# Performance work log

Hardware: AMD Instinct MI355X
Metric: run time of the kernel (lower is better)

Reference implementation:

```python
import jax, jax.numpy as jnp
import numpy as np

GAMMA = 267.52  # gyromagnetic ratio constant used as default in forward


def make_laplacian_kernel(vox=(1.0, 1.0, 1.0)):
    vx, vy, vz = vox
    mx, my, mz = 1.0 / vx ** 2, 1.0 / vy ** 2, 1.0 / vz ** 2
    mv = -2.0 * (mx + my + mz)
    k = np.zeros((3, 3, 3), dtype=np.float32)
    # layout matches the torch conv_op nested list: k[d, h, w]
    k[0, 1, 1] = mz
    k[2, 1, 1] = mz
    k[1, 0, 1] = mx
    k[1, 2, 1] = mx
    k[1, 1, 0] = my
    k[1, 1, 2] = my
    k[1, 1, 1] = mv
    return jnp.asarray(k)[None, None]  # [O=1, I=1, 3, 3, 3]


def lg(x, kernel):
    # conv3d, stride 1, padding 1 (SAME for 3^3 kernel), NCDHW
    out = jax.lax.conv_general_dilated(
        x, kernel, window_strides=(1, 1, 1), padding=[(1, 1)] * 3,
        dimension_numbers=('NCDHW', 'OIDHW', 'NCDHW'))
    # zero the boundary slices along each spatial dim (matches LG)
    out = out.at[:, :, 0, :, :].set(0.0).at[:, :, -1, :, :].set(0.0)
    out = out.at[:, :, :, 0, :].set(0.0).at[:, :, :, -1, :].set(0.0)
    out = out.at[:, :, :, :, 0].set(0.0).at[:, :, :, :, -1].set(0.0)
    return out


def setup_inputs() -> dict:
    key = jax.random.key(0)
    k1, k2 = jax.random.split(key)
    B, C, H, W, D = 2, 1, 256, 256, 128
    phi = jax.random.normal(k1, (B, C, H, W, D), dtype=jnp.float32)
    lfs = jax.random.normal(k2, (B, C, H, W, D), dtype=jnp.float32) * 0.01
    mask = jnp.ones((B, C, H, W, D), dtype=jnp.float32)
    TE = jax.random.uniform(jax.random.fold_in(key, 1), (B,), dtype=jnp.float32) * 0.02 + 0.005
    B0 = jnp.full((1,), 3.0, dtype=jnp.float32)
    kernel = make_laplacian_kernel((1.0, 1.0, 1.0))
    return {"phi": phi, "lfs": lfs, "mask": mask, "TE": TE, "B0": B0, "kernel": kernel}


def reference(phi, lfs, mask, TE, B0, kernel):
    expPhi_r = jnp.cos(phi)
    expPhi_i = jnp.sin(phi)
    a_r = lg(expPhi_r, kernel)
    a_i = lg(expPhi_i, kernel)
    b_i = (a_i * expPhi_r - a_r * expPhi_i) * mask
    te = TE[:, None, None, None, None]  # broadcast over [B,1,H,W,D]
    b_i = -b_i / (B0 * te * GAMMA)
    d_i = lg(lfs, kernel) * mask
    return (b_i, d_i)
```

## Files before the change

kernel.cpp:

```cpp
#include <hip/hip_runtime.h>

#define GAMMA_F 267.52f
typedef float v4f __attribute__((ext_vector_type(4)));

constexpr int H = 256, W = 256, D = 128;
constexpr int WT = 8;
constexpr int HS = 16;
constexpr int LW = WT + 2;
constexpr long long sW = D;
constexpr long long sH = (long long)W * D;
constexpr long long sB = (long long)H * (long long)W * D;

__global__ __launch_bounds__(256, 4) void lot_lds_v2(
    const float* __restrict__ phi,
    const float* __restrict__ lfs,
    const float* __restrict__ mask,
    const float* __restrict__ TE,
    const float* __restrict__ B0,
    const float* __restrict__ kern,
    float* __restrict__ out_b,
    float* __restrict__ out_d)
{
    __shared__ float Ssin[3][LW][D];
    __shared__ float Scos[3][LW][D];

    const int tid = threadIdx.x;
    const int q   = tid & 31;
    const int wr  = tid >> 5;
    const int w0  = blockIdx.x * WT;
    const int h0  = blockIdx.y * HS;
    const int b   = blockIdx.z;
    const int w   = w0 + wr;
    const int d0  = q * 4;
    const int lwc = wr + 1;

    const long long colBase = (long long)b * sB + (long long)w * sW + d0;

    const float kHc = kern[4];
    const float kWc = kern[10];
    const float kDc = kern[12];
    const float kCc = kern[13];
    const float scale = -1.0f / (B0[0] * TE[b] * GAMMA_F);

    const bool haloLo  = (wr == 0)      && (w0 > 0);
    const bool haloHi  = (wr == WT - 1) && (w0 + WT < W);
    const bool hasHalo = haloLo || haloHi;
    const long long haloOff = haloLo ? -sW : sW;
    const int  haloLw  = haloLo ? 0 : (LW - 1);

    #define PHI_LOAD(hh, P, PH)                                              \
    do {                                                                     \
        const int _h = (hh);                                                 \
        if (_h >= 0 && _h < H) {                                             \
            const long long _r = colBase + (long long)_h * sH;               \
            P = *(const v4f*)(phi + _r);                                     \
            if (hasHalo) PH = *(const v4f*)(phi + _r + haloOff);             \
        }                                                                    \
    } while (0)

    #define SINCOS_STORE(SLOT, P, PH, SN, CS)                                \
    do {                                                                     \
        const int _s = (SLOT);                                               \
        SN[0] = __sinf(P.x); SN[1] = __sinf(P.y);                            \
        SN[2] = __sinf(P.z); SN[3] = __sinf(P.w);                            \
        CS[0] = __cosf(P.x); CS[1] = __cosf(P.y);                            \
        CS[2] = __cosf(P.z); CS[3] = __cosf(P.w);                            \
        v4f _vs = {SN[0], SN[1], SN[2], SN[3]};                              \
        v4f _vc = {CS[0], CS[1], CS[2], CS[3]};                              \
        *(v4f*)&Ssin[_s][lwc][d0] = _vs;                                     \
        *(v4f*)&Scos[_s][lwc][d0] = _vc;                                     \
        if (hasHalo) {                                                       \
            v4f _hs = {__sinf(PH.x), __sinf(PH.y), __sinf(PH.z), __sinf(PH.w)}; \
            v4f _hc = {__cosf(PH.x), __cosf(PH.y), __cosf(PH.z), __cosf(PH.w)}; \
            *(v4f*)&Ssin[_s][haloLw][d0] = _hs;                              \
            *(v4f*)&Scos[_s][haloLw][d0] = _hc;                              \
        }                                                                    \
    } while (0)

    #define LFS_LOAD(hh, F)                                                  \
    do {                                                                     \
        const int _h = (hh);                                                 \
        if (_h >= 0 && _h < H) {                                             \
            const long long _r = colBase + (long long)_h * sH;               \
            const v4f _l = *(const v4f*)(lfs + _r);                          \
            F[1] = _l.x; F[2] = _l.y; F[3] = _l.z; F[4] = _l.w;              \
            F[0] = (d0 > 0)     ? lfs[_r - 1] : 0.f;                         \
            F[5] = (d0 + 4 < D) ? lfs[_r + 4] : 0.f;                         \
        } else {                                                             \
            _Pragma("unroll")                                                \
            for (int _j = 0; _j < 6; ++_j) F[_j] = 0.f;                      \
        }                                                                    \
    } while (0)

    v4f pN  = {0.f, 0.f, 0.f, 0.f}, pNH  = {0.f, 0.f, 0.f, 0.f};
    float snC[4], csC[4], snT[4], csT[4];
    float FA[6], FB[6], FC[6];

    PHI_LOAD(h0 - 1, pN, pNH);
    SINCOS_STORE(0, pN, pNH, snT, csT);
    PHI_LOAD(h0, pN, pNH);
    SINCOS_STORE(1, pN, pNH, snC, csC);
    LFS_LOAD(h0 - 1, FA);
    LFS_LOAD(h0,     FB);
    PHI_LOAD(h0 + 1, pN, pNH);

    int sm = 0, sc = 1, sp = 2;

    for (int i = 0; i < HS; ++i) {
        const int h = h0 + i;

        SINCOS_STORE(sp, pN, pNH, snT, csT);
        LFS_LOAD(h + 1, FC);
        __syncthreads();

        v4f pN2 = pN, pN2H = pNH;
        PHI_LOAD(h + 2, pN2, pN2H);

        const long long r = colBase + (long long)h * sH;
        if (h == 0 || h == H - 1 || w == 0 || w == W - 1) {
            const v4f z = {0.f, 0.f, 0.f, 0.f};
            __builtin_nontemporal_store(z, (v4f*)(out_b + r));
            __builtin_nontemporal_store(z, (v4f*)(out_d + r));
        } else {
            const v4f swm = *(const v4f*)&Ssin[sc][lwc - 1][d0];
            const v4f swp = *(const v4f*)&Ssin[sc][lwc + 1][d0];
            const v4f shm = *(const v4f*)&Ssin[sm][lwc][d0];
            const v4f shp = *(const v4f*)&Ssin[sp][lwc][d0];
            const v4f cwm = *(const v4f*)&Scos[sc][lwc - 1][d0];
            const v4f cwp = *(const v4f*)&Scos[sc][lwc + 1][d0];
            const v4f chm = *(const v4f*)&Scos[sm][lwc][d0];
            const v4f chp = *(const v4f*)&Scos[sp][lwc][d0];

            const float snL = __shfl_up(snC[3], 1, 32);
            const float snR = __shfl_down(snC[0], 1, 32);
            const float csL = __shfl_up(csC[3], 1, 32);
            const float csR = __shfl_down(csC[0], 1, 32);
            const float snx[6] = {snL, snC[0], snC[1], snC[2], snC[3], snR};
            const float csx[6] = {csL, csC[0], csC[1], csC[2], csC[3], csR};

            const v4f lw0 = *(const v4f*)(lfs + r - sW);
            const v4f lw1 = *(const v4f*)(lfs + r + sW);
            const v4f mk  = *(const v4f*)(mask + r);
            const float lwv0[4] = {lw0.x, lw0.y, lw0.z, lw0.w};
            const float lwv1[4] = {lw1.x, lw1.y, lw1.z, lw1.w};
            const float mkv[4]  = {mk.x, mk.y, mk.z, mk.w};
            const float swmv[4] = {swm.x, swm.y, swm.z, swm.w};
            const float swpv[4] = {swp.x, swp.y, swp.z, swp.w};
            const float shmv[4] = {shm.x, shm.y, shm.z, shm.w};
            const float shpv[4] = {shp.x, shp.y, shp.z, shp.w};
            const float cwmv[4] = {cwm.x, cwm.y, cwm.z, cwm.w};
            const float cwpv[4] = {cwp.x, cwp.y, cwp.z, cwp.w};
            const float chmv[4] = {chm.x, chm.y, chm.z, chm.w};
            const float chpv[4] = {chp.x, chp.y, chp.z, chp.w};

            float ob[4], od[4];
            #pragma unroll
            for (int j = 0; j < 4; ++j) {
                const float se = snx[j + 1], ce = csx[j + 1];
                const float a_r = kCc * ce
                    + kDc * (csx[j] + csx[j + 2])
                    + kWc * (cwmv[j] + cwpv[j])
                    + kHc * (chmv[j] + chpv[j]);
                const float a_i = kCc * se
                    + kDc * (snx[j] + snx[j + 2])
                    + kWc * (swmv[j] + swpv[j])
                    + kHc * (shmv[j] + shpv[j]);
                float bi = (a_i * ce - a_r * se) * mkv[j] * scale;

                const float lap = kCc * FB[j + 1]
                    + kDc * (FB[j] + FB[j + 2])
                    + kWc * (lwv0[j] + lwv1[j])
                    + kHc * (FA[j + 1] + FC[j + 1]);
                float dv = lap * mkv[j];

                const int d = d0 + j;
                if (d == 0 || d == D - 1) { bi = 0.f; dv = 0.f; }
                ob[j] = bi; od[j] = dv;
            }
            const v4f vb = {ob[0], ob[1], ob[2], ob[3]};
            const v4f vd = {od[0], od[1], od[2], od[3]};
            __builtin_nontemporal_store(vb, (v4f*)(out_b + r));
            __builtin_nontemporal_store(vd, (v4f*)(out_d + r));
        }

        #pragma unroll
        for (int j2 = 0; j2 < 4; ++j2) { snC[j2] = snT[j2]; csC[j2] = csT[j2]; }
        #pragma unroll
        for (int j2 = 0; j2 < 6; ++j2) { FA[j2] = FB[j2]; FB[j2] = FC[j2]; }
        pN = pN2; pNH = pN2H;
        const int t = sm; sm = sc; sc = sp; sp = t;

        __syncthreads();
    }

    #undef PHI_LOAD
    #undef SINCOS_STORE
    #undef LFS_LOAD
}

extern "C" void kernel_launch(void* const* d_in, const int* in_sizes, int n_in,
                              void* d_out, int out_size, void* d_ws, size_t ws_size,
                              hipStream_t stream) {
    const float* phi  = (const float*)d_in[0];
    const float* lfs  = (const float*)d_in[1];
    const float* mask = (const float*)d_in[2];
    const float* TE   = (const float*)d_in[3];
    const float* B0   = (const float*)d_in[4];
    const float* kern = (const float*)d_in[5];

    float* out_b = (float*)d_out;
    float* out_d = out_b + sB * 2;

    dim3 grid(W / WT, H / HS, 2);
    dim3 block(256);
    hipLaunchKernelGGL(lot_lds_v2, grid, block, 0, stream,
                       phi, lfs, mask, TE, B0, kern, out_b, out_d);
}
```

Measured before the change: 65.90 us.

## Keep H-neighbour sincos in registers and use a single barrier per row

The H-direction neighbours' sin/cos now live in per-thread rolling registers, so LDS holds only the centre row for W-neighbour exchange. A 3-slot ring lets each iteration get by with one __syncthreads instead of two. The lfs prefetch moves one row further ahead and the loop is fully unrolled. The H strip per block is halved and the occupancy hint raised to 5 waves. The smaller strip adds more halo-row reloads and sin/cos recomputation, and the extra live registers may pressure the new launch bound.

```diff
diff --git a/kernel.cpp b/kernel.cpp
--- a/kernel.cpp
+++ b/kernel.cpp
@@ -5,13 +5,13 @@
 
 constexpr int H = 256, W = 256, D = 128;
 constexpr int WT = 8;
-constexpr int HS = 16;
+constexpr int HS = 8;
 constexpr int LW = WT + 2;
 constexpr long long sW = D;
 constexpr long long sH = (long long)W * D;
 constexpr long long sB = (long long)H * (long long)W * D;
 
-__global__ __launch_bounds__(256, 4) void lot_lds_v2(
+__global__ __launch_bounds__(256, 5) void lot_lds_v3(
     const float* __restrict__ phi,
     const float* __restrict__ lfs,
     const float* __restrict__ mask,
@@ -58,13 +58,18 @@
         }                                                                    \
     } while (0)
 
-    #define SINCOS_STORE(SLOT, P, PH, SN, CS)                                \
-    do {                                                                     \
-        const int _s = (SLOT);                                               \
+    #define SINCOS_REG(P, SN, CS)                                            \
+    do {                                                                     \
         SN[0] = __sinf(P.x); SN[1] = __sinf(P.y);                            \
         SN[2] = __sinf(P.z); SN[3] = __sinf(P.w);                            \
         CS[0] = __cosf(P.x); CS[1] = __cosf(P.y);                            \
         CS[2] = __cosf(P.z); CS[3] = __cosf(P.w);                            \
+    } while (0)
+
+    #define SINCOS_STORE(SLOT, P, PH, SN, CS)                                \
+    do {                                                                     \
+        const int _s = (SLOT);                                               \
+        SINCOS_REG(P, SN, CS);                                               \
         v4f _vs = {SN[0], SN[1], SN[2], SN[3]};                              \
         v4f _vc = {CS[0], CS[1], CS[2], CS[3]};                              \
         *(v4f*)&Ssin[_s][lwc][d0] = _vs;                                     \
@@ -92,29 +97,33 @@
         }                                                                    \
     } while (0)
 
-    v4f pN  = {0.f, 0.f, 0.f, 0.f}, pNH  = {0.f, 0.f, 0.f, 0.f};
-    float snC[4], csC[4], snT[4], csT[4];
+    v4f pN = {0.f, 0.f, 0.f, 0.f}, pNH = {0.f, 0.f, 0.f, 0.f};
+    float snM[4], csM[4], snC[4], csC[4], snP[4], csP[4];
     float FA[6], FB[6], FC[6];
 
     PHI_LOAD(h0 - 1, pN, pNH);
-    SINCOS_STORE(0, pN, pNH, snT, csT);
+    SINCOS_REG(pN, snM, csM);
     PHI_LOAD(h0, pN, pNH);
-    SINCOS_STORE(1, pN, pNH, snC, csC);
+    SINCOS_STORE(0, pN, pNH, snC, csC);
     LFS_LOAD(h0 - 1, FA);
     LFS_LOAD(h0,     FB);
     PHI_LOAD(h0 + 1, pN, pNH);
-
-    int sm = 0, sc = 1, sp = 2;
-
+    LFS_LOAD(h0 + 1, FC);
+
+    #pragma unroll
     for (int i = 0; i < HS; ++i) {
         const int h = h0 + i;
-
-        SINCOS_STORE(sp, pN, pNH, snT, csT);
-        LFS_LOAD(h + 1, FC);
-        __syncthreads();
+        const int slotW = (i + 1) % 3;
+        const int slotR = i % 3;
+
+        SINCOS_STORE(slotW, pN, pNH, snP, csP);
 
         v4f pN2 = pN, pN2H = pNH;
         PHI_LOAD(h + 2, pN2, pN2H);
+        float FC2[6];
+        LFS_LOAD(h + 2, FC2);
+
+        __syncthreads();
 
         const long long r = colBase + (long long)h * sH;
         if (h == 0 || h == H - 1 || w == 0 || w == W - 1) {
@@ -122,14 +131,10 @@
             __builtin_nontemporal_store(z, (v4f*)(out_b + r));
             __builtin_nontemporal_store(z, (v4f*)(out_d + r));
         } else {
-            const v4f swm = *(const v4f*)&Ssin[sc][lwc - 1][d0];
-            const v4f swp = *(const v4f*)&Ssin[sc][lwc + 1][d0];
-            const v4f shm = *(const v4f*)&Ssin[sm][lwc][d0];
-            const v4f shp = *(const v4f*)&Ssin[sp][lwc][d0];
-            const v4f cwm = *(const v4f*)&Scos[sc][lwc - 1][d0];
-            const v4f cwp = *(const v4f*)&Scos[sc][lwc + 1][d0];
-            const v4f chm = *(const v4f*)&Scos[sm][lwc][d0];
-            const v4f chp = *(const v4f*)&Scos[sp][lwc][d0];
+            const v4f swm = *(const v4f*)&Ssin[slotR][lwc - 1][d0];
+            const v4f swp = *(const v4f*)&Ssin[slotR][lwc + 1][d0];
+            const v4f cwm = *(const v4f*)&Scos[slotR][lwc - 1][d0];
+            const v4f cwp = *(const v4f*)&Scos[slotR][lwc + 1][d0];
 
             const float snL = __shfl_up(snC[3], 1, 32);
             const float snR = __shfl_down(snC[0], 1, 32);
@@ -146,12 +151,8 @@
             const float mkv[4]  = {mk.x, mk.y, mk.z, mk.w};
             const float swmv[4] = {swm.x, swm.y, swm.z, swm.w};
             const float swpv[4] = {swp.x, swp.y, swp.z, swp.w};
-            const float shmv[4] = {shm.x, shm.y, shm.z, shm.w};
-            const float shpv[4] = {shp.x, shp.y, shp.z, shp.w};
             const float cwmv[4] = {cwm.x, cwm.y, cwm.z, cwm.w};
             const float cwpv[4] = {cwp.x, cwp.y, cwp.z, cwp.w};
-            const float chmv[4] = {chm.x, chm.y, chm.z, chm.w};
-            const float chpv[4] = {chp.x, chp.y, chp.z, chp.w};
 
             float ob[4], od[4];
             #pragma unroll
@@ -160,11 +161,11 @@
                 const float a_r = kCc * ce
                     + kDc * (csx[j] + csx[j + 2])
                     + kWc * (cwmv[j] + cwpv[j])
-                    + kHc * (chmv[j] + chpv[j]);
+                    + kHc * (csM[j] + csP[j]);
                 const float a_i = kCc * se
                     + kDc * (snx[j] + snx[j + 2])
                     + kWc * (swmv[j] + swpv[j])
-                    + kHc * (shmv[j] + shpv[j]);
+                    + kHc * (snM[j] + snP[j]);
                 float bi = (a_i * ce - a_r * se) * mkv[j] * scale;
 
                 const float lap = kCc * FB[j + 1]
@@ -184,16 +185,19 @@
         }
 
         #pragma unroll
-        for (int j2 = 0; j2 < 4; ++j2) { snC[j2] = snT[j2]; csC[j2] = csT[j2]; }
+        for (int j2 = 0; j2 < 4; ++j2) {
+            snM[j2] = snC[j2]; csM[j2] = csC[j2];
+            snC[j2] = snP[j2]; csC[j2] = csP[j2];
+        }
         #pragma unroll
-        for (int j2 = 0; j2 < 6; ++j2) { FA[j2] = FB[j2]; FB[j2] = FC[j2]; }
+        for (int j2 = 0; j2 < 6; ++j2) {
+            FA[j2] = FB[j2]; FB[j2] = FC[j2]; FC[j2] = FC2[j2];
+        }
         pN = pN2; pNH = pN2H;
-        const int t = sm; sm = sc; sc = sp; sp = t;
-
-        __syncthreads();
     }
 
     #undef PHI_LOAD
+    #undef SINCOS_REG
     #undef SINCOS_STORE
     #undef LFS_LOAD
 }
@@ -213,6 +217,6 @@
 
     dim3 grid(W / WT, H / HS, 2);
     dim3 block(256);
-    hipLaunchKernelGGL(lot_lds_v2, grid, block, 0, stream,
+    hipLaunchKernelGGL(lot_lds_v3, grid, block, 0, stream,
                        phi, lfs, mask, TE, B0, kern, out_b, out_d);
 }
```

Result: slower. 85.49 us (+29.7%).
